# Kernel tuning notes

Hardware: AMD Instinct MI355X
Metric: run time of the kernel (lower is better)

The kernel has to match this reference:

```python
import jax, jax.numpy as jnp
import numpy as np

N_NODES = 50000
N_EDGES = 600000
D_NODE_IN = 32
D_EDGE_IN = 16
H = 128
D_OUT = 2
N_PASSES = 5
LN_EPS = 1e-6  # flax LayerNorm default


def _dense(key, fan_in, fan_out, scale=0.05):
    return (jax.random.normal(key, (fan_in, fan_out), dtype=jnp.float32) * scale)


def setup_inputs() -> dict:
    key = jax.random.key(0)
    ks = jax.random.split(key, 16)
    inp = {
        "nodes": jax.random.normal(ks[0], (N_NODES, D_NODE_IN), dtype=jnp.float32),
        "edges": jax.random.normal(ks[1], (N_EDGES, D_EDGE_IN), dtype=jnp.float32),
        "senders": jax.random.randint(ks[2], (N_EDGES,), 0, N_NODES, dtype=jnp.int32),
        "receivers": jax.random.randint(ks[3], (N_EDGES,), 0, N_NODES, dtype=jnp.int32),
        # node encoder ReluMLP [128,128]
        "enc_n_W0": _dense(ks[4], D_NODE_IN, H), "enc_n_b0": jnp.zeros((H,), jnp.float32),
        "enc_n_W1": _dense(ks[5], H, H), "enc_n_b1": jnp.zeros((H,), jnp.float32),
        # edge encoder ReluMLP [128,128]
        "enc_e_W0": _dense(ks[6], D_EDGE_IN, H), "enc_e_b0": jnp.zeros((H,), jnp.float32),
        "enc_e_W1": _dense(ks[7], H, H), "enc_e_b1": jnp.zeros((H,), jnp.float32),
        # weight-tied LinearMessagePassingLayer params
        "W_msg": _dense(ks[8], H + H, H),                 # Dense(no bias) on concat(sender_feat, edge)
        "node_W0": _dense(ks[9], H + H, H), "node_b0": jnp.zeros((H,), jnp.float32),
        "node_W1": _dense(ks[10], H, H), "node_b1": jnp.zeros((H,), jnp.float32),
        "W_node": _dense(ks[11], H, H),                   # residual projection, no bias
        "ln_g": jnp.ones((H,), jnp.float32), "ln_b": jnp.zeros((H,), jnp.float32),
        # node decoder ReluMLP [128,2]
        "dec_W0": _dense(ks[12], H, H), "dec_b0": jnp.zeros((H,), jnp.float32),
        "dec_W1": _dense(ks[13], H, D_OUT), "dec_b1": jnp.zeros((D_OUT,), jnp.float32),
    }
    return inp


def _relu_mlp(x, layers):
    # Dense+ReLU for all but last layer; last layer linear.
    n = len(layers)
    for i, (W, b) in enumerate(layers):
        x = x @ W + b
        if i < n - 1:
            x = jax.nn.relu(x)
    return x


def _layer_norm(x, g, b):
    mu = jnp.mean(x, axis=-1, keepdims=True)
    var = jnp.var(x, axis=-1, keepdims=True)
    return (x - mu) * jax.lax.rsqrt(var + LN_EPS) * g + b


def reference(nodes, edges, senders, receivers,
              enc_n_W0, enc_n_b0, enc_n_W1, enc_n_b1,
              enc_e_W0, enc_e_b0, enc_e_W1, enc_e_b1,
              W_msg, node_W0, node_b0, node_W1, node_b1,
              W_node, ln_g, ln_b,
              dec_W0, dec_b0, dec_W1, dec_b1):
    n = _relu_mlp(nodes, [(enc_n_W0, enc_n_b0), (enc_n_W1, enc_n_b1)])  # [N,H]
    e = _relu_mlp(edges, [(enc_e_W0, enc_e_b0), (enc_e_W1, enc_e_b1)])  # [E,H]
    total_nodes = n.shape[0]

    for _ in range(N_PASSES):  # weight-tied process block
        sender_features = n[senders]                                    # gather [E,H]
        msg_in = jnp.concatenate([sender_features, e], axis=-1)         # [E,2H]
        messages = msg_in @ W_msg                                       # [E,H]
        agg = jax.ops.segment_sum(messages, receivers, num_segments=total_nodes)
        node_in = jnp.concatenate([n, agg], axis=-1)                    # [N,2H]
        nodes_out = _relu_mlp(node_in, [(node_W0, node_b0), (node_W1, node_b1)])
        n = _layer_norm(n @ W_node + nodes_out, ln_g, ln_b)

    return _relu_mlp(n, [(dec_W0, dec_b0), (dec_W1, dec_b1)])           # [N,2]
```

## Files before the change

kernel.cpp:

```cpp
#include <hip/hip_runtime.h>

#define DEVFN __device__ __forceinline__

namespace {

constexpr int NN = 50000;
constexpr int NE = 600000;
constexpr int H  = 128;
constexpr float LN_EPS = 1e-6f;

typedef _Float16 f16x8 __attribute__((ext_vector_type(8)));
typedef _Float16 f16x4 __attribute__((ext_vector_type(4)));
typedef float f32x4 __attribute__((ext_vector_type(4)));

DEVFN void mm_block(const float* xsrow, int pitch, int K,
                    const float* __restrict__ W, int c0, float (&acc)[8][4]) {
  for (int k = 0; k < K; k += 4) {
    float4 w0 = *(const float4*)(W + (size_t)(k + 0) * H + c0);
    float4 w1 = *(const float4*)(W + (size_t)(k + 1) * H + c0);
    float4 w2 = *(const float4*)(W + (size_t)(k + 2) * H + c0);
    float4 w3 = *(const float4*)(W + (size_t)(k + 3) * H + c0);
#pragma unroll
    for (int r = 0; r < 8; ++r) {
      float4 a = *(const float4*)(xsrow + r * pitch + k);
      acc[r][0] += a.x * w0.x; acc[r][0] += a.y * w1.x; acc[r][0] += a.z * w2.x; acc[r][0] += a.w * w3.x;
      acc[r][1] += a.x * w0.y; acc[r][1] += a.y * w1.y; acc[r][1] += a.z * w2.y; acc[r][1] += a.w * w3.y;
      acc[r][2] += a.x * w0.z; acc[r][2] += a.y * w1.z; acc[r][2] += a.z * w2.z; acc[r][2] += a.w * w3.z;
      acc[r][3] += a.x * w0.w; acc[r][3] += a.y * w1.w; acc[r][3] += a.z * w2.w; acc[r][3] += a.w * w3.w;
    }
  }
}

DEVFN void linear_body(const float* __restrict__ x, const float* __restrict__ W,
                       float* __restrict__ y, int r0, int R, int t, float* xs) {
  {
    const int r = t & 31, q = t >> 5;
    int row = r0 + r;
    if (row >= R) row = R - 1;
    const float* src = &x[(size_t)row * H + q * 32];
#pragma unroll
    for (int j = 0; j < 8; ++j)
      *(float4*)&xs[r * 132 + q * 32 + j * 4] = *(const float4*)&src[j * 4];
  }
  __syncthreads();
  const int c0 = (t & 31) * 4;
  const int rbase = (t >> 5) * 8;
  float acc[8][4];
#pragma unroll
  for (int r = 0; r < 8; ++r) { acc[r][0] = 0.f; acc[r][1] = 0.f; acc[r][2] = 0.f; acc[r][3] = 0.f; }
  mm_block(&xs[rbase * 132], 132, H, W, c0, acc);
#pragma unroll
  for (int r = 0; r < 8; ++r) {
    int row = r0 + rbase + r;
    if (row < R)
      *(float4*)&y[(size_t)row * H + c0] =
          make_float4(acc[r][0], acc[r][1], acc[r][2], acc[r][3]);
  }
}

template <int K_IN>
__global__ __launch_bounds__(128) void encoder_kernel(
    const float* __restrict__ x, const float* __restrict__ W0,
    const float* __restrict__ b0, const float* __restrict__ W1,
    const float* __restrict__ b1, _Float16* __restrict__ outp, int R) {
  constexpr int PIN = K_IN + 4;
  __shared__ float xs[32 * PIN];
  __shared__ float hs[32 * 132];
  const int t = threadIdx.x;
  const int r0 = blockIdx.x * 32;

  const int nvec = 32 * K_IN / 4;
  for (int i = t; i < nvec; i += 128) {
    int rr = i / (K_IN / 4);
    int kk = (i % (K_IN / 4)) * 4;
    int row = r0 + rr;
    float4 v = make_float4(0.f, 0.f, 0.f, 0.f);
    if (row < R) v = *(const float4*)&x[(size_t)row * K_IN + kk];
    *(float4*)&xs[rr * PIN + kk] = v;
  }
  __syncthreads();

  const int c0 = (t & 31) * 4;
  const int rbase = (t >> 5) * 8;
  float acc[8][4];
  {
    float4 bb = *(const float4*)&b0[c0];
#pragma unroll
    for (int r = 0; r < 8; ++r) { acc[r][0] = bb.x; acc[r][1] = bb.y; acc[r][2] = bb.z; acc[r][3] = bb.w; }
  }
  mm_block(&xs[rbase * PIN], PIN, K_IN, W0, c0, acc);
#pragma unroll
  for (int r = 0; r < 8; ++r) {
    float4 h;
    h.x = fmaxf(acc[r][0], 0.f); h.y = fmaxf(acc[r][1], 0.f);
    h.z = fmaxf(acc[r][2], 0.f); h.w = fmaxf(acc[r][3], 0.f);
    *(float4*)&hs[(rbase + r) * 132 + c0] = h;
  }
  __syncthreads();
  {
    float4 bb = *(const float4*)&b1[c0];
#pragma unroll
    for (int r = 0; r < 8; ++r) { acc[r][0] = bb.x; acc[r][1] = bb.y; acc[r][2] = bb.z; acc[r][3] = bb.w; }
  }
  mm_block(&hs[rbase * 132], 132, H, W1, c0, acc);
#pragma unroll
  for (int r = 0; r < 8; ++r) {
    int row = r0 + rbase + r;
    if (row < R) {
      f16x4 pk = {(_Float16)acc[r][0], (_Float16)acc[r][1],
                  (_Float16)acc[r][2], (_Float16)acc[r][3]};
      *(f16x4*)&outp[(size_t)row * H + c0] = pk;
    }
  }
}

__global__ __launch_bounds__(128) void fold1_kernel(
    const float* __restrict__ Wb, const float* __restrict__ Wt,
    const float* __restrict__ W0b, float* __restrict__ T,
    float* __restrict__ Wf) {
  __shared__ float xs[32 * 132];
  const float* x = (blockIdx.x < 4) ? Wb : Wt;
  float* y = (blockIdx.x < 4) ? T : Wf;
  linear_body(x, W0b, y, (blockIdx.x & 3) * 32, 128, threadIdx.x, xs);
}

__global__ __launch_bounds__(128) void fold2_kernel(
    const float* __restrict__ W1e, const float* __restrict__ b1e,
    const float* __restrict__ T, float* __restrict__ Wc2,
    float* __restrict__ bc2) {
  __shared__ float xs[32 * 132];
  if (blockIdx.x < 4) {
    linear_body(W1e, T, Wc2, blockIdx.x * 32, 128, threadIdx.x, xs);
  } else {
    int j = threadIdx.x;
    float s = 0.f;
    for (int k = 0; k < H; ++k) s += b1e[k] * T[(size_t)k * H + j];
    bc2[j] = s;
  }
}

__global__ __launch_bounds__(64) void prepack4_kernel(
    const float* __restrict__ s0, const float* __restrict__ s1,
    const float* __restrict__ s2, const float* __restrict__ s3,
    _Float16* __restrict__ pkBase) {
  const int z = blockIdx.z;
  const float* W = (z == 0) ? s0 : (z == 1) ? s1 : (z == 2) ? s2 : s3;
  _Float16* pk = pkBase + (size_t)z * 128 * H;
  const int ks = blockIdx.x, ct = blockIdx.y, l = threadIdx.x;
  const int kbase = ks * 32 + (l >> 4) * 8;
  const int col = ct * 16 + (l & 15);
  _Float16 tmp[8];
#pragma unroll
  for (int j = 0; j < 8; ++j)
    tmp[j] = (_Float16)W[(size_t)(kbase + j) * H + col];
  *(f16x8*)&pk[((size_t)((ks * 8 + ct) * 64) + l) * 8] = *(f16x8*)tmp;
}

__global__ __launch_bounds__(64) void prepack_w0e_kernel(
    const float* __restrict__ W0e, _Float16* __restrict__ pk) {
  const int ct = blockIdx.x, l = threadIdx.x;
  const int quad = l >> 4;
  const int col = ct * 16 + (l & 15);
  _Float16 tmp[8];
#pragma unroll
  for (int j = 0; j < 8; ++j) {
    int k = quad * 8 + j;
    tmp[j] = (quad < 2) ? (_Float16)W0e[(size_t)k * H + col] : (_Float16)0.f;
  }
  *(f16x8*)&pk[((size_t)(ct * 64) + l) * 8] = *(f16x8*)tmp;
}

__global__ __launch_bounds__(256) void hist_kernel(const int* __restrict__ recv,
                                                   int* __restrict__ cnt) {
  int i = blockIdx.x * 256 + threadIdx.x;
  if (i < NE) atomicAdd(&cnt[recv[i]], 1);
}

__global__ __launch_bounds__(256) void scan1_kernel(const int* __restrict__ cnt,
                                                    int* __restrict__ excl,
                                                    int* __restrict__ part) {
  __shared__ int s[256];
  int t = threadIdx.x;
  int i = blockIdx.x * 256 + t;
  int v = (i < NN) ? cnt[i] : 0;
  s[t] = v;
  __syncthreads();
  for (int off = 1; off < 256; off <<= 1) {
    int x = (t >= off) ? s[t - off] : 0;
    __syncthreads();
    s[t] += x;
    __syncthreads();
  }
  if (i < NN) excl[i] = s[t] - v;
  if (t == 255) part[blockIdx.x] = s[255];
}

__global__ __launch_bounds__(256) void scan2_kernel(int* __restrict__ part, int nb) {
  __shared__ int s[256];
  int t = threadIdx.x;
  int v = (t < nb) ? part[t] : 0;
  s[t] = v;
  __syncthreads();
  for (int off = 1; off < 256; off <<= 1) {
    int x = (t >= off) ? s[t - off] : 0;
    __syncthreads();
    s[t] += x;
    __syncthreads();
  }
  if (t < nb) part[t] = s[t] - v;
}

__global__ __launch_bounds__(256) void scan3_kernel(int* __restrict__ excl,
                                                    const int* __restrict__ part,
                                                    int* __restrict__ cursor) {
  int i = blockIdx.x * 256 + threadIdx.x;
  if (i < NN) {
    int e = excl[i] + part[i >> 8];
    excl[i] = e;
    cursor[i] = e;
  }
}

__global__ __launch_bounds__(256) void scatter_permute_kernel(
    const int* __restrict__ senders, const int* __restrict__ recv,
    int* __restrict__ cursor, const float* __restrict__ edges,
    int* __restrict__ sendp, _Float16* __restrict__ edgesP16) {
  const int t = threadIdx.x;
  const int i = blockIdx.x * 64 + (t >> 2);
  if (i >= NE) return;
  const int sub = t & 3;
  int pos = 0;
  if (sub == 0) pos = atomicAdd(&cursor[recv[i]], 1);
  pos = __shfl(pos, (t & 63) & ~3);
  if (sub == 0) sendp[pos] = senders[i];
  float4 v = *(const float4*)&edges[(size_t)i * 16 + sub * 4];
  f16x4 h = {(_Float16)v.x, (_Float16)v.y, (_Float16)v.z, (_Float16)v.w};
  *(f16x4*)&edgesP16[(size_t)pos * 16 + sub * 4] = h;
}

__global__ __launch_bounds__(256) void hs_mfma_kernel(
    const _Float16* __restrict__ edgesP16, const int* __restrict__ start,
    const int* __restrict__ endc, const _Float16* __restrict__ pkW0e,
    const float* __restrict__ b0e, float* __restrict__ Hs) {
  const int t = threadIdx.x;
  const int wave = t >> 6, lane = t & 63;
  const int v = blockIdx.x * 4 + wave;
  const int quad = lane >> 4, m16 = lane & 15;
  const int j0 = start[v];
  const int deg = endc[v] - j0;

  float binit[8];
#pragma unroll
  for (int ct = 0; ct < 8; ++ct) binit[ct] = b0e[ct * 16 + m16];
  f16x8 bfrag[8];
#pragma unroll
  for (int ct = 0; ct < 8; ++ct)
    bfrag[ct] = *(const f16x8*)&pkW0e[((size_t)(ct * 64) + lane) * 8];

  float rsum[8][4];
#pragma unroll
  for (int ct = 0; ct < 8; ++ct)
#pragma unroll
    for (int q = 0; q < 4; ++q) rsum[ct][q] = 0.f;

  for (int base = 0; base < deg; base += 16) {
    f16x8 a = {};
    if (quad < 2 && base + m16 < deg)
      a = *(const f16x8*)&edgesP16[(size_t)(j0 + base + m16) * 16 + quad * 8];
#pragma unroll
    for (int ct = 0; ct < 8; ++ct) {
      f32x4 acc = (f32x4){binit[ct], binit[ct], binit[ct], binit[ct]};
      acc = __builtin_amdgcn_mfma_f32_16x16x32_f16(a, bfrag[ct], acc, 0, 0, 0);
#pragma unroll
      for (int q = 0; q < 4; ++q) {
        int row = quad * 4 + q;
        float hv = fmaxf(acc[q], 0.f);
        rsum[ct][q] += (base + row < deg) ? hv : 0.f;
      }
    }
  }
#pragma unroll
  for (int ct = 0; ct < 8; ++ct) {
    float s = (rsum[ct][0] + rsum[ct][1]) + (rsum[ct][2] + rsum[ct][3]);
    s += __shfl_xor(s, 16);
    s += __shfl_xor(s, 32);
    if (lane < 16) Hs[(size_t)v * H + ct * 16 + lane] = s;
  }
}

__global__ __launch_bounds__(128) void blinpack_kernel(
    const float* __restrict__ Hs, const float* __restrict__ Wc2,
    const float* __restrict__ bc2, const int* __restrict__ start,
    const int* __restrict__ endc, _Float16* __restrict__ B2pk) {
  __shared__ float xs[32 * 132];
  const int t = threadIdx.x;
  const int r0 = blockIdx.x * 32;
  {
    const int r = t & 31, q = t >> 5;
    int row = r0 + r;
    if (row >= NN) row = NN - 1;
    const float* src = &Hs[(size_t)row * H + q * 32];
#pragma unroll
    for (int j = 0; j < 8; ++j)
      *(float4*)&xs[r * 132 + q * 32 + j * 4] = *(const float4*)&src[j * 4];
  }
  __syncthreads();
  const int c0 = (t & 31) * 4;
  const int rbase = (t >> 5) * 8;
  const float4 bc4 = *(const float4*)&bc2[c0];
  float acc[8][4];
#pragma unroll
  for (int r = 0; r < 8; ++r) {
    int row = r0 + rbase + r;
    if (row >= NN) row = NN - 1;
    float deg = (float)(endc[row] - start[row]);
    acc[r][0] = deg * bc4.x; acc[r][1] = deg * bc4.y;
    acc[r][2] = deg * bc4.z; acc[r][3] = deg * bc4.w;
  }
  mm_block(&xs[rbase * 132], 132, H, Wc2, c0, acc);
  __syncthreads();
#pragma unroll
  for (int r = 0; r < 8; ++r)
    *(float4*)&xs[(rbase + r) * 132 + c0] =
        make_float4(acc[r][0], acc[r][1], acc[r][2], acc[r][3]);
  __syncthreads();
  const int half = t >> 6, l = t & 63;
  const int tile = blockIdx.x * 2 + half;
  const int rb = half * 16 + (l >> 4) * 4;
  const int col = l & 15;
  _Float16 tmp[32];
#pragma unroll
  for (int ct = 0; ct < 8; ++ct)
#pragma unroll
    for (int q = 0; q < 4; ++q)
      tmp[ct * 4 + q] = (_Float16)xs[(rb + q) * 132 + ct * 16 + col];
  _Float16* dst = &B2pk[((size_t)tile * 64 + l) * 32];
#pragma unroll
  for (int i = 0; i < 4; ++i)
    *(f16x8*)(dst + i * 8) = *(f16x8*)(tmp + i * 8);
}

__global__ __launch_bounds__(256) void gather_kernel(
    const _Float16* __restrict__ n16, const int* __restrict__ start,
    const int* __restrict__ endc, const int* __restrict__ sendp,
    _Float16* __restrict__ S) {
  const int t = threadIdx.x;
  const int v = blockIdx.x * 4 + (t >> 6);
  const int lane = t & 63;
  const int grp = lane >> 4;
  const int c = (lane & 15) * 8;
  float a[8] = {0.f, 0.f, 0.f, 0.f, 0.f, 0.f, 0.f, 0.f};
  const int e = endc[v];
  int j = start[v];
  for (; j + 7 < e; j += 8) {
    int s0 = sendp[j + grp];
    int s1 = sendp[j + 4 + grp];
    f16x8 p0 = *(const f16x8*)&n16[(size_t)s0 * H + c];
    f16x8 p1 = *(const f16x8*)&n16[(size_t)s1 * H + c];
#pragma unroll
    for (int i = 0; i < 8; ++i) a[i] += (float)p0[i] + (float)p1[i];
  }
  for (; j < e; j += 4) {
    int jj = j + grp;
    if (jj < e) {
      int s0 = sendp[jj];
      f16x8 p0 = *(const f16x8*)&n16[(size_t)s0 * H + c];
#pragma unroll
      for (int i = 0; i < 8; ++i) a[i] += (float)p0[i];
    }
  }
#pragma unroll
  for (int i = 0; i < 8; ++i) {
    a[i] += __shfl_xor(a[i], 16);
    a[i] += __shfl_xor(a[i], 32);
  }
  if (lane < 16) {
    f16x8 o;
#pragma unroll
    for (int i = 0; i < 8; ++i) o[i] = (_Float16)a[i];
    *(f16x8*)&S[(size_t)v * H + c] = o;
  }
}

__global__ __launch_bounds__(256) void node_mfma_kernel(
    const _Float16* __restrict__ n16, const _Float16* __restrict__ S16,
    const _Float16* __restrict__ B2pk,
    const _Float16* __restrict__ pkW0t, const _Float16* __restrict__ pkWf,
    const float* __restrict__ b0,
    const _Float16* __restrict__ pkW1, const _Float16* __restrict__ pkWn,
    const float* __restrict__ b1,
    const float* __restrict__ ln_g, const float* __restrict__ ln_b,
    _Float16* __restrict__ nout) {
  __shared__ _Float16 lds[4][16 * 136];
  const int t = threadIdx.x;
  const int wave = t >> 6, lane = t & 63;
  const int row0 = blockIdx.x * 64 + wave * 16;
  const int quad = lane >> 4, m16 = lane & 15;
  _Float16* hlds = &lds[wave][0];

  int arow = row0 + m16;
  if (arow >= NN) arow = NN - 1;
  const _Float16* nrow = &n16[(size_t)arow * H + quad * 8];
  const _Float16* srow = &S16[(size_t)arow * H + quad * 8];
  f16x8 an[4], as[4];
#pragma unroll
  for (int ks = 0; ks < 4; ++ks) {
    an[ks] = *(const f16x8*)(nrow + ks * 32);
    as[ks] = *(const f16x8*)(srow + ks * 32);
  }

  const int tile = blockIdx.x * 4 + wave;
  const _Float16* b2l = &B2pk[((size_t)tile * 64 + lane) * 32];
  f32x4 acc[8];
#pragma unroll
  for (int ct = 0; ct < 8; ++ct) {
    float bb = b0[ct * 16 + m16];
    f16x4 bv = *(const f16x4*)(b2l + ct * 4);
    acc[ct] = (f32x4){bb + (float)bv[0], bb + (float)bv[1],
                      bb + (float)bv[2], bb + (float)bv[3]};
  }
#pragma unroll
  for (int ks = 0; ks < 4; ++ks) {
    const _Float16* bp0 = pkW0t + ((size_t)ks * 8 * 64 + lane) * 8;
    const _Float16* bpf = pkWf + ((size_t)ks * 8 * 64 + lane) * 8;
#pragma unroll
    for (int ct = 0; ct < 8; ++ct) {
      f16x8 bw0 = *(const f16x8*)(bp0 + ct * 512);
      acc[ct] = __builtin_amdgcn_mfma_f32_16x16x32_f16(an[ks], bw0, acc[ct], 0, 0, 0);
      f16x8 bwf = *(const f16x8*)(bpf + ct * 512);
      acc[ct] = __builtin_amdgcn_mfma_f32_16x16x32_f16(as[ks], bwf, acc[ct], 0, 0, 0);
    }
  }
#pragma unroll
  for (int ct = 0; ct < 8; ++ct) {
#pragma unroll
    for (int q = 0; q < 4; ++q)
      hlds[(quad * 4 + q) * 136 + ct * 16 + m16] =
          (_Float16)fmaxf(acc[ct][q], 0.f);
  }
  __syncthreads();

  const _Float16* hrow = &hlds[m16 * 136 + quad * 8];
  f32x4 acc2[8];
#pragma unroll
  for (int ct = 0; ct < 8; ++ct) {
    float bb = b1[ct * 16 + m16];
    acc2[ct] = (f32x4){bb, bb, bb, bb};
  }
#pragma unroll
  for (int ks = 0; ks < 4; ++ks) {
    f16x8 ah = *(const f16x8*)(hrow + ks * 32);
    const _Float16* bp1 = pkW1 + ((size_t)ks * 8 * 64 + lane) * 8;
    const _Float16* bpn = pkWn + ((size_t)ks * 8 * 64 + lane) * 8;
#pragma unroll
    for (int ct = 0; ct < 8; ++ct) {
      f16x8 b1f = *(const f16x8*)(bp1 + ct * 512);
      acc2[ct] = __builtin_amdgcn_mfma_f32_16x16x32_f16(ah, b1f, acc2[ct], 0, 0, 0);
      f16x8 bnf = *(const f16x8*)(bpn + ct * 512);
      acc2[ct] = __builtin_amdgcn_mfma_f32_16x16x32_f16(an[ks], bnf, acc2[ct], 0, 0, 0);
    }
  }

  float gv[8], bv[8];
#pragma unroll
  for (int ct = 0; ct < 8; ++ct) {
    gv[ct] = ln_g[ct * 16 + m16];
    bv[ct] = ln_b[ct * 16 + m16];
  }
  __syncthreads();
#pragma unroll
  for (int q = 0; q < 4; ++q) {
    float s1 = 0.f, s2 = 0.f;
#pragma unroll
    for (int ct = 0; ct < 8; ++ct) {
      float v = acc2[ct][q];
      s1 += v; s2 += v * v;
    }
#pragma unroll
    for (int m = 1; m <= 8; m <<= 1) {
      s1 += __shfl_xor(s1, m);
      s2 += __shfl_xor(s2, m);
    }
    float mu = s1 * (1.f / 128.f);
    float var = s2 * (1.f / 128.f) - mu * mu;
    float rs = rsqrtf(var + LN_EPS);
#pragma unroll
    for (int ct = 0; ct < 8; ++ct) {
      float o = (acc2[ct][q] - mu) * rs * gv[ct] + bv[ct];
      hlds[(quad * 4 + q) * 136 + ct * 16 + m16] = (_Float16)o;
    }
  }
  __syncthreads();

  {
    int lr = lane >> 2;
    int cc = (lane & 3) * 32;
    const _Float16* src = &hlds[lr * 136 + cc];
    int orow = row0 + lr;
    if (orow < NN) {
      _Float16* dst = &nout[(size_t)orow * H + cc];
      *(f16x8*)(dst + 0)  = *(const f16x8*)(src + 0);
      *(f16x8*)(dst + 8)  = *(const f16x8*)(src + 8);
      *(f16x8*)(dst + 16) = *(const f16x8*)(src + 16);
      *(f16x8*)(dst + 24) = *(const f16x8*)(src + 24);
    }
  }
}

__global__ __launch_bounds__(128) void decode_kernel(
    const _Float16* __restrict__ n, const float* __restrict__ W0,
    const float* __restrict__ b0, const float* __restrict__ W1,
    const float* __restrict__ b1, float* __restrict__ out) {
  __shared__ float xs[32 * 132];
  __shared__ float hs[32 * 132];
  const int t = threadIdx.x;
  const int r0 = blockIdx.x * 32;
  {
    const int r = t & 31, q = t >> 5;
    int row = r0 + r;
    if (row >= NN) row = NN - 1;
    const _Float16* src = &n[(size_t)row * H + q * 32];
#pragma unroll
    for (int j = 0; j < 4; ++j) {
      f16x8 v8 = *(const f16x8*)&src[j * 8];
#pragma unroll
      for (int i = 0; i < 8; ++i)
        xs[r * 132 + q * 32 + j * 8 + i] = (float)v8[i];
    }
  }
  __syncthreads();
  const int c0 = (t & 31) * 4;
  const int rbase = (t >> 5) * 8;
  float acc[8][4];
  {
    float4 bb = *(const float4*)&b0[c0];
#pragma unroll
    for (int r = 0; r < 8; ++r) { acc[r][0] = bb.x; acc[r][1] = bb.y; acc[r][2] = bb.z; acc[r][3] = bb.w; }
  }
  mm_block(&xs[rbase * 132], 132, H, W0, c0, acc);
#pragma unroll
  for (int r = 0; r < 8; ++r) {
    float4 h;
    h.x = fmaxf(acc[r][0], 0.f); h.y = fmaxf(acc[r][1], 0.f);
    h.z = fmaxf(acc[r][2], 0.f); h.w = fmaxf(acc[r][3], 0.f);
    *(float4*)&hs[(rbase + r) * 132 + c0] = h;
  }
  __syncthreads();
  if (t < 64) {
    int r = t >> 1, c = t & 1;
    float s = b1[c];
    for (int k = 0; k < H; ++k) s += hs[r * 132 + k] * W1[k * 2 + c];
    int row = r0 + r;
    if (row < NN) out[(size_t)row * 2 + c] = s;
  }
}

__global__ __launch_bounds__(256) void zero_kernel(float4* __restrict__ p, int n4) {
  int i = blockIdx.x * 256 + threadIdx.x;
  if (i < n4) p[i] = make_float4(0.f, 0.f, 0.f, 0.f);
}

}

extern "C" void kernel_launch(void* const* d_in, const int* in_sizes, int n_in,
                              void* d_out, int out_size, void* d_ws, size_t ws_size,
                              hipStream_t stream) {
  const float* nodes     = (const float*)d_in[0];
  const float* edges     = (const float*)d_in[1];
  const int*   senders   = (const int*)d_in[2];
  const int*   receivers = (const int*)d_in[3];
  const float* enc_n_W0 = (const float*)d_in[4];
  const float* enc_n_b0 = (const float*)d_in[5];
  const float* enc_n_W1 = (const float*)d_in[6];
  const float* enc_n_b1 = (const float*)d_in[7];
  const float* enc_e_W0 = (const float*)d_in[8];
  const float* enc_e_b0 = (const float*)d_in[9];
  const float* enc_e_W1 = (const float*)d_in[10];
  const float* enc_e_b1 = (const float*)d_in[11];
  const float* W_msg    = (const float*)d_in[12];
  const float* node_W0  = (const float*)d_in[13];
  const float* node_b0  = (const float*)d_in[14];
  const float* node_W1  = (const float*)d_in[15];
  const float* node_b1  = (const float*)d_in[16];
  const float* W_node   = (const float*)d_in[17];
  const float* ln_g     = (const float*)d_in[18];
  const float* ln_b     = (const float*)d_in[19];
  const float* dec_W0   = (const float*)d_in[20];
  const float* dec_b0   = (const float*)d_in[21];
  const float* dec_W1   = (const float*)d_in[22];
  const float* dec_b1   = (const float*)d_in[23];
  float* out = (float*)d_out;

  const float* Wt  = W_msg;
  const float* Wb  = W_msg + 128 * H;
  const float* W0t = node_W0;
  const float* W0b = node_W0 + 128 * H;

  const int mfmaBlocks = (NN + 63) / 64;
  const int nTiles     = mfmaBlocks * 4;

  float* Hs     = (float*)d_ws;
  float* T      = Hs + (size_t)NN * H;
  float* Wc2    = T + 128 * H;
  float* Wf32   = Wc2 + 128 * H;
  float* bc2    = Wf32 + 128 * H;
  _Float16* edgesP16 = (_Float16*)(bc2 + 128);
  _Float16* n16a  = edgesP16 + (size_t)NE * 16;
  _Float16* n16b  = n16a + (size_t)NN * H;
  _Float16* S16   = n16b + (size_t)NN * H;
  _Float16* B2pk  = S16 + (size_t)NN * H;
  _Float16* pkAll = B2pk + (size_t)nTiles * 64 * 32;
  _Float16* pkW0t = pkAll;
  _Float16* pkWf  = pkAll + 1 * 128 * H;
  _Float16* pkW1  = pkAll + 2 * 128 * H;
  _Float16* pkWn  = pkAll + 3 * 128 * H;
  _Float16* pkW0e = pkAll + 4 * 128 * H;
  int* cnt    = (int*)(pkW0e + 4096);
  int* excl   = cnt + NN;
  int* cursor = excl + NN;
  int* part   = cursor + NN;
  int* sendp  = part + 256;

  const int nodeBlocks = (NN + 31) / 32;
  const int scanBlocks = (NN + 255) / 256;
  const int neBlocks   = (NE + 255) / 256;

  zero_kernel<<<(NN / 4 + 255) / 256, 256, 0, stream>>>((float4*)cnt, NN / 4);
  hist_kernel<<<neBlocks, 256, 0, stream>>>(receivers, cnt);
  scan1_kernel<<<scanBlocks, 256, 0, stream>>>(cnt, excl, part);
  scan2_kernel<<<1, 256, 0, stream>>>(part, scanBlocks);
  scan3_kernel<<<scanBlocks, 256, 0, stream>>>(excl, part, cursor);
  scatter_permute_kernel<<<(NE + 63) / 64, 256, 0, stream>>>(
      senders, receivers, cursor, edges, sendp, edgesP16);

  fold1_kernel<<<8, 128, 0, stream>>>(Wb, Wt, W0b, T, Wf32);
  fold2_kernel<<<5, 128, 0, stream>>>(enc_e_W1, enc_e_b1, T, Wc2, bc2);
  prepack4_kernel<<<dim3(4, 8, 4), 64, 0, stream>>>(W0t, Wf32, node_W1, W_node, pkAll);
  prepack_w0e_kernel<<<8, 64, 0, stream>>>(enc_e_W0, pkW0e);

  encoder_kernel<32><<<nodeBlocks, 128, 0, stream>>>(
      nodes, enc_n_W0, enc_n_b0, enc_n_W1, enc_n_b1, n16a, NN);
  hs_mfma_kernel<<<NN / 4, 256, 0, stream>>>(
      edgesP16, excl, cursor, pkW0e, enc_e_b0, Hs);
  blinpack_kernel<<<nodeBlocks, 128, 0, stream>>>(Hs, Wc2, bc2, excl, cursor, B2pk);

  _Float16* ncur = n16a;
  _Float16* nnxt = n16b;
  for (int p = 0; p < 5; ++p) {
    gather_kernel<<<NN / 4, 256, 0, stream>>>(ncur, excl, cursor, sendp, S16);
    node_mfma_kernel<<<mfmaBlocks, 256, 0, stream>>>(
        ncur, S16, B2pk, pkW0t, pkWf, node_b0, pkW1, pkWn, node_b1,
        ln_g, ln_b, nnxt);
    _Float16* tmp = ncur; ncur = nnxt; nnxt = tmp;
  }

  decode_kernel<<<nodeBlocks, 128, 0, stream>>>(ncur, dec_W0, dec_b0, dec_W1, dec_b1, out);
}
```

Baseline: 628.0 us.

## Move node encoder, blinpack and decoder matmuls onto fp16 MFMA

```diff
diff --git a/kernel.cpp b/kernel.cpp
--- a/kernel.cpp
+++ b/kernel.cpp
@@ -55,62 +55,6 @@
     if (row < R)
       *(float4*)&y[(size_t)row * H + c0] =
           make_float4(acc[r][0], acc[r][1], acc[r][2], acc[r][3]);
-  }
-}
-
-template <int K_IN>
-__global__ __launch_bounds__(128) void encoder_kernel(
-    const float* __restrict__ x, const float* __restrict__ W0,
-    const float* __restrict__ b0, const float* __restrict__ W1,
-    const float* __restrict__ b1, _Float16* __restrict__ outp, int R) {
-  constexpr int PIN = K_IN + 4;
-  __shared__ float xs[32 * PIN];
-  __shared__ float hs[32 * 132];
-  const int t = threadIdx.x;
-  const int r0 = blockIdx.x * 32;
-
-  const int nvec = 32 * K_IN / 4;
-  for (int i = t; i < nvec; i += 128) {
-    int rr = i / (K_IN / 4);
-    int kk = (i % (K_IN / 4)) * 4;
-    int row = r0 + rr;
-    float4 v = make_float4(0.f, 0.f, 0.f, 0.f);
-    if (row < R) v = *(const float4*)&x[(size_t)row * K_IN + kk];
-    *(float4*)&xs[rr * PIN + kk] = v;
-  }
-  __syncthreads();
-
-  const int c0 = (t & 31) * 4;
-  const int rbase = (t >> 5) * 8;
-  float acc[8][4];
-  {
-    float4 bb = *(const float4*)&b0[c0];
-#pragma unroll
-    for (int r = 0; r < 8; ++r) { acc[r][0] = bb.x; acc[r][1] = bb.y; acc[r][2] = bb.z; acc[r][3] = bb.w; }
-  }
-  mm_block(&xs[rbase * PIN], PIN, K_IN, W0, c0, acc);
-#pragma unroll
-  for (int r = 0; r < 8; ++r) {
-    float4 h;
-    h.x = fmaxf(acc[r][0], 0.f); h.y = fmaxf(acc[r][1], 0.f);
-    h.z = fmaxf(acc[r][2], 0.f); h.w = fmaxf(acc[r][3], 0.f);
-    *(float4*)&hs[(rbase + r) * 132 + c0] = h;
-  }
-  __syncthreads();
-  {
-    float4 bb = *(const float4*)&b1[c0];
-#pragma unroll
-    for (int r = 0; r < 8; ++r) { acc[r][0] = bb.x; acc[r][1] = bb.y; acc[r][2] = bb.z; acc[r][3] = bb.w; }
-  }
-  mm_block(&hs[rbase * 132], 132, H, W1, c0, acc);
-#pragma unroll
-  for (int r = 0; r < 8; ++r) {
-    int row = r0 + rbase + r;
-    if (row < R) {
-      f16x4 pk = {(_Float16)acc[r][0], (_Float16)acc[r][1],
-                  (_Float16)acc[r][2], (_Float16)acc[r][3]};
-      *(f16x4*)&outp[(size_t)row * H + c0] = pk;
-    }
   }
 }
 
@@ -139,12 +83,14 @@
   }
 }
 
-__global__ __launch_bounds__(64) void prepack4_kernel(
+__global__ __launch_bounds__(64) void prepack7_kernel(
     const float* __restrict__ s0, const float* __restrict__ s1,
     const float* __restrict__ s2, const float* __restrict__ s3,
-    _Float16* __restrict__ pkBase) {
+    const float* __restrict__ s4, const float* __restrict__ s5,
+    const float* __restrict__ s6, _Float16* __restrict__ pkBase) {
   const int z = blockIdx.z;
-  const float* W = (z == 0) ? s0 : (z == 1) ? s1 : (z == 2) ? s2 : s3;
+  const float* W = (z == 0) ? s0 : (z == 1) ? s1 : (z == 2) ? s2 :
+                   (z == 3) ? s3 : (z == 4) ? s4 : (z == 5) ? s5 : s6;
   _Float16* pk = pkBase + (size_t)z * 128 * H;
   const int ks = blockIdx.x, ct = blockIdx.y, l = threadIdx.x;
   const int kbase = ks * 32 + (l >> 4) * 8;
@@ -167,6 +113,18 @@
     int k = quad * 8 + j;
     tmp[j] = (quad < 2) ? (_Float16)W0e[(size_t)k * H + col] : (_Float16)0.f;
   }
+  *(f16x8*)&pk[((size_t)(ct * 64) + l) * 8] = *(f16x8*)tmp;
+}
+
+__global__ __launch_bounds__(64) void prepack_k32_kernel(
+    const float* __restrict__ W, _Float16* __restrict__ pk) {
+  const int ct = blockIdx.x, l = threadIdx.x;
+  const int quad = l >> 4;
+  const int col = ct * 16 + (l & 15);
+  _Float16 tmp[8];
+#pragma unroll
+  for (int j = 0; j < 8; ++j)
+    tmp[j] = (_Float16)W[(size_t)(quad * 8 + j) * H + col];
   *(f16x8*)&pk[((size_t)(ct * 64) + l) * 8] = *(f16x8*)tmp;
 }
 
@@ -238,6 +196,79 @@
   *(f16x4*)&edgesP16[(size_t)pos * 16 + sub * 4] = h;
 }
 
+__global__ __launch_bounds__(256) void encoder_mfma_kernel(
+    const float* __restrict__ x, const float* __restrict__ b0,
+    const float* __restrict__ b1, const _Float16* __restrict__ pkEW0,
+    const _Float16* __restrict__ pkEW1, _Float16* __restrict__ outp) {
+  __shared__ _Float16 lds[4][16 * 136];
+  const int t = threadIdx.x;
+  const int wave = t >> 6, lane = t & 63;
+  const int row0 = blockIdx.x * 64 + wave * 16;
+  const int quad = lane >> 4, m16 = lane & 15;
+  _Float16* hlds = &lds[wave][0];
+
+  int arow = row0 + m16;
+  if (arow >= NN) arow = NN - 1;
+  f16x8 a0;
+  {
+    const float* src = &x[(size_t)arow * 32 + quad * 8];
+    float4 v0 = *(const float4*)(src);
+    float4 v1 = *(const float4*)(src + 4);
+    a0[0] = (_Float16)v0.x; a0[1] = (_Float16)v0.y;
+    a0[2] = (_Float16)v0.z; a0[3] = (_Float16)v0.w;
+    a0[4] = (_Float16)v1.x; a0[5] = (_Float16)v1.y;
+    a0[6] = (_Float16)v1.z; a0[7] = (_Float16)v1.w;
+  }
+#pragma unroll
+  for (int ct = 0; ct < 8; ++ct) {
+    float bb = b0[ct * 16 + m16];
+    f32x4 acc = (f32x4){bb, bb, bb, bb};
+    acc = __builtin_amdgcn_mfma_f32_16x16x32_f16(
+        a0, *(const f16x8*)&pkEW0[((size_t)(ct * 64) + lane) * 8], acc, 0, 0, 0);
+#pragma unroll
+    for (int q = 0; q < 4; ++q)
+      hlds[(quad * 4 + q) * 136 + ct * 16 + m16] = (_Float16)fmaxf(acc[q], 0.f);
+  }
+  __syncthreads();
+  const _Float16* hrow = &hlds[m16 * 136 + quad * 8];
+  f16x8 ah[4];
+#pragma unroll
+  for (int ks = 0; ks < 4; ++ks) ah[ks] = *(const f16x8*)(hrow + ks * 32);
+  f32x4 acc2[8];
+#pragma unroll
+  for (int ct = 0; ct < 8; ++ct) {
+    float bb = b1[ct * 16 + m16];
+    acc2[ct] = (f32x4){bb, bb, bb, bb};
+  }
+#pragma unroll
+  for (int ks = 0; ks < 4; ++ks) {
+    const _Float16* bp = pkEW1 + ((size_t)ks * 8 * 64 + lane) * 8;
+#pragma unroll
+    for (int ct = 0; ct < 8; ++ct)
+      acc2[ct] = __builtin_amdgcn_mfma_f32_16x16x32_f16(
+          ah[ks], *(const f16x8*)(bp + ct * 512), acc2[ct], 0, 0, 0);
+  }
+  __syncthreads();
+#pragma unroll
+  for (int ct = 0; ct < 8; ++ct)
+#pragma unroll
+    for (int q = 0; q < 4; ++q)
+      hlds[(quad * 4 + q) * 136 + ct * 16 + m16] = (_Float16)acc2[ct][q];
+  __syncthreads();
+  {
+    int lr = lane >> 2, cc = (lane & 3) * 32;
+    int orow = row0 + lr;
+    if (orow < NN) {
+      const _Float16* src = &hlds[lr * 136 + cc];
+      _Float16* dst = &outp[(size_t)orow * H + cc];
+      *(f16x8*)(dst + 0)  = *(const f16x8*)(src + 0);
+      *(f16x8*)(dst + 8)  = *(const f16x8*)(src + 8);
+      *(f16x8*)(dst + 16) = *(const f16x8*)(src + 16);
+      *(f16x8*)(dst + 24) = *(const f16x8*)(src + 24);
+    }
+  }
+}
+
 __global__ __launch_bounds__(256) void hs_mfma_kernel(
     const _Float16* __restrict__ edgesP16, const int* __restrict__ start,
     const int* __restrict__ endc, const _Float16* __restrict__ pkW0e,
@@ -288,53 +319,56 @@
   }
 }
 
-__global__ __launch_bounds__(128) void blinpack_kernel(
-    const float* __restrict__ Hs, const float* __restrict__ Wc2,
+__global__ __launch_bounds__(256) void blinpack_mfma_kernel(
+    const float* __restrict__ Hs, const _Float16* __restrict__ pkWc2,
     const float* __restrict__ bc2, const int* __restrict__ start,
     const int* __restrict__ endc, _Float16* __restrict__ B2pk) {
-  __shared__ float xs[32 * 132];
   const int t = threadIdx.x;
-  const int r0 = blockIdx.x * 32;
-  {
-    const int r = t & 31, q = t >> 5;
-    int row = r0 + r;
-    if (row >= NN) row = NN - 1;
-    const float* src = &Hs[(size_t)row * H + q * 32];
-#pragma unroll
-    for (int j = 0; j < 8; ++j)
-      *(float4*)&xs[r * 132 + q * 32 + j * 4] = *(const float4*)&src[j * 4];
-  }
-  __syncthreads();
-  const int c0 = (t & 31) * 4;
-  const int rbase = (t >> 5) * 8;
-  const float4 bc4 = *(const float4*)&bc2[c0];
-  float acc[8][4];
-#pragma unroll
-  for (int r = 0; r < 8; ++r) {
-    int row = r0 + rbase + r;
-    if (row >= NN) row = NN - 1;
-    float deg = (float)(endc[row] - start[row]);
-    acc[r][0] = deg * bc4.x; acc[r][1] = deg * bc4.y;
-    acc[r][2] = deg * bc4.z; acc[r][3] = deg * bc4.w;
-  }
-  mm_block(&xs[rbase * 132], 132, H, Wc2, c0, acc);
-  __syncthreads();
-#pragma unroll
-  for (int r = 0; r < 8; ++r)
-    *(float4*)&xs[(rbase + r) * 132 + c0] =
-        make_float4(acc[r][0], acc[r][1], acc[r][2], acc[r][3]);
-  __syncthreads();
-  const int half = t >> 6, l = t & 63;
-  const int tile = blockIdx.x * 2 + half;
-  const int rb = half * 16 + (l >> 4) * 4;
-  const int col = l & 15;
+  const int wave = t >> 6, lane = t & 63;
+  const int tile = blockIdx.x * 4 + wave;
+  const int row0 = tile * 16;
+  const int quad = lane >> 4, m16 = lane & 15;
+  int arow = row0 + m16;
+  if (arow >= NN) arow = NN - 1;
+  f16x8 ah[4];
+#pragma unroll
+  for (int ks = 0; ks < 4; ++ks) {
+    const float* src = &Hs[(size_t)arow * H + ks * 32 + quad * 8];
+    float4 v0 = *(const float4*)src;
+    float4 v1 = *(const float4*)(src + 4);
+    f16x8 a;
+    a[0] = (_Float16)v0.x; a[1] = (_Float16)v0.y;
+    a[2] = (_Float16)v0.z; a[3] = (_Float16)v0.w;
+    a[4] = (_Float16)v1.x; a[5] = (_Float16)v1.y;
+    a[6] = (_Float16)v1.z; a[7] = (_Float16)v1.w;
+    ah[ks] = a;
+  }
+  float degq[4];
+#pragma unroll
+  for (int q = 0; q < 4; ++q) {
+    int r = row0 + quad * 4 + q;
+    degq[q] = (r < NN) ? (float)(endc[r] - start[r]) : 0.f;
+  }
+  f32x4 acc[8];
+#pragma unroll
+  for (int ct = 0; ct < 8; ++ct) {
+    float bcv = bc2[ct * 16 + m16];
+    acc[ct] = (f32x4){degq[0] * bcv, degq[1] * bcv, degq[2] * bcv, degq[3] * bcv};
+  }
+#pragma unroll
+  for (int ks = 0; ks < 4; ++ks) {
+    const _Float16* bp = pkWc2 + ((size_t)ks * 8 * 64 + lane) * 8;
+#pragma unroll
+    for (int ct = 0; ct < 8; ++ct)
+      acc[ct] = __builtin_amdgcn_mfma_f32_16x16x32_f16(
+          ah[ks], *(const f16x8*)(bp + ct * 512), acc[ct], 0, 0, 0);
+  }
   _Float16 tmp[32];
 #pragma unroll
   for (int ct = 0; ct < 8; ++ct)
 #pragma unroll
-    for (int q = 0; q < 4; ++q)
-      tmp[ct * 4 + q] = (_Float16)xs[(rb + q) * 132 + ct * 16 + col];
-  _Float16* dst = &B2pk[((size_t)tile * 64 + l) * 32];
+    for (int q = 0; q < 4; ++q) tmp[ct * 4 + q] = (_Float16)acc[ct][q];
+  _Float16* dst = &B2pk[((size_t)tile * 64 + lane) * 32];
 #pragma unroll
   for (int i = 0; i < 4; ++i)
     *(f16x8*)(dst + i * 8) = *(f16x8*)(tmp + i * 8);
@@ -507,51 +541,62 @@
   }
 }
 
-__global__ __launch_bounds__(128) void decode_kernel(
-    const _Float16* __restrict__ n, const float* __restrict__ W0,
-    const float* __restrict__ b0, const float* __restrict__ W1,
+__global__ __launch_bounds__(256) void decode_mfma_kernel(
+    const _Float16* __restrict__ n, const float* __restrict__ b0,
+    const _Float16* __restrict__ pkDW0, const float* __restrict__ W1,
     const float* __restrict__ b1, float* __restrict__ out) {
-  __shared__ float xs[32 * 132];
-  __shared__ float hs[32 * 132];
   const int t = threadIdx.x;
-  const int r0 = blockIdx.x * 32;
-  {
-    const int r = t & 31, q = t >> 5;
-    int row = r0 + r;
-    if (row >= NN) row = NN - 1;
-    const _Float16* src = &n[(size_t)row * H + q * 32];
-#pragma unroll
-    for (int j = 0; j < 4; ++j) {
-      f16x8 v8 = *(const f16x8*)&src[j * 8];
-#pragma unroll
-      for (int i = 0; i < 8; ++i)
-        xs[r * 132 + q * 32 + j * 8 + i] = (float)v8[i];
-    }
-  }
-  __syncthreads();
-  const int c0 = (t & 31) * 4;
-  const int rbase = (t >> 5) * 8;
-  float acc[8][4];
-  {
-    float4 bb = *(const float4*)&b0[c0];
-#pragma unroll
-    for (int r = 0; r < 8; ++r) { acc[r][0] = bb.x; acc[r][1] = bb.y; acc[r][2] = bb.z; acc[r][3] = bb.w; }
-  }
-  mm_block(&xs[rbase * 132], 132, H, W0, c0, acc);
-#pragma unroll
-  for (int r = 0; r < 8; ++r) {
-    float4 h;
-    h.x = fmaxf(acc[r][0], 0.f); h.y = fmaxf(acc[r][1], 0.f);
-    h.z = fmaxf(acc[r][2], 0.f); h.w = fmaxf(acc[r][3], 0.f);
-    *(float4*)&hs[(rbase + r) * 132 + c0] = h;
-  }
-  __syncthreads();
-  if (t < 64) {
-    int r = t >> 1, c = t & 1;
-    float s = b1[c];
-    for (int k = 0; k < H; ++k) s += hs[r * 132 + k] * W1[k * 2 + c];
-    int row = r0 + r;
-    if (row < NN) out[(size_t)row * 2 + c] = s;
+  const int wave = t >> 6, lane = t & 63;
+  const int row0 = blockIdx.x * 64 + wave * 16;
+  const int quad = lane >> 4, m16 = lane & 15;
+  int arow = row0 + m16;
+  if (arow >= NN) arow = NN - 1;
+  const _Float16* nrow = &n[(size_t)arow * H + quad * 8];
+  f16x8 an[4];
+#pragma unroll
+  for (int ks = 0; ks < 4; ++ks) an[ks] = *(const f16x8*)(nrow + ks * 32);
+  f32x4 acc[8];
+#pragma unroll
+  for (int ct = 0; ct < 8; ++ct) {
+    float bb = b0[ct * 16 + m16];
+    acc[ct] = (f32x4){bb, bb, bb, bb};
+  }
+#pragma unroll
+  for (int ks = 0; ks < 4; ++ks) {
+    const _Float16* bp = pkDW0 + ((size_t)ks * 8 * 64 + lane) * 8;
+#pragma unroll
+    for (int ct = 0; ct < 8; ++ct)
+      acc[ct] = __builtin_amdgcn_mfma_f32_16x16x32_f16(
+          an[ks], *(const f16x8*)(bp + ct * 512), acc[ct], 0, 0, 0);
+  }
+  float s0[4] = {0.f, 0.f, 0.f, 0.f}, s1[4] = {0.f, 0.f, 0.f, 0.f};
+#pragma unroll
+  for (int ct = 0; ct < 8; ++ct) {
+    const float2 w = *(const float2*)&W1[(size_t)(ct * 16 + m16) * 2];
+#pragma unroll
+    for (int q = 0; q < 4; ++q) {
+      float h = fmaxf(acc[ct][q], 0.f);
+      s0[q] += h * w.x;
+      s1[q] += h * w.y;
+    }
+  }
+#pragma unroll
+  for (int q = 0; q < 4; ++q) {
+#pragma unroll
+    for (int m = 1; m <= 8; m <<= 1) {
+      s0[q] += __shfl_xor(s0[q], m);
+      s1[q] += __shfl_xor(s1[q], m);
+    }
+  }
+  if (m16 == 0) {
+#pragma unroll
+    for (int q = 0; q < 4; ++q) {
+      int r = row0 + quad * 4 + q;
+      if (r < NN) {
+        out[(size_t)r * 2 + 0] = s0[q] + b1[0];
+        out[(size_t)r * 2 + 1] = s1[q] + b1[1];
+      }
+    }
   }
 }
 
@@ -614,14 +659,17 @@
   _Float16* pkWf  = pkAll + 1 * 128 * H;
   _Float16* pkW1  = pkAll + 2 * 128 * H;
   _Float16* pkWn  = pkAll + 3 * 128 * H;
-  _Float16* pkW0e = pkAll + 4 * 128 * H;
-  int* cnt    = (int*)(pkW0e + 4096);
+  _Float16* pkEW1 = pkAll + 4 * 128 * H;
+  _Float16* pkDW0 = pkAll + 5 * 128 * H;
+  _Float16* pkWc2 = pkAll + 6 * 128 * H;
+  _Float16* pkW0e = pkAll + 7 * 128 * H;
+  _Float16* pkEW0 = pkW0e + 4096;
+  int* cnt    = (int*)(pkEW0 + 4096);
   int* excl   = cnt + NN;
   int* cursor = excl + NN;
   int* part   = cursor + NN;
   int* sendp  = part + 256;
 
-  const int nodeBlocks = (NN + 31) / 32;
   const int scanBlocks = (NN + 255) / 256;
   const int neBlocks   = (NE + 255) / 256;
 
@@ -635,14 +683,17 @@
 
   fold1_kernel<<<8, 128, 0, stream>>>(Wb, Wt, W0b, T, Wf32);
   fold2_kernel<<<5, 128, 0, stream>>>(enc_e_W1, enc_e_b1, T, Wc2, bc2);
-  prepack4_kernel<<<dim3(4, 8, 4), 64, 0, stream>>>(W0t, Wf32, node_W1, W_node, pkAll);
+  prepack7_kernel<<<dim3(4, 8, 7), 64, 0, stream>>>(
+      W0t, Wf32, node_W1, W_node, enc_n_W1, dec_W0, Wc2, pkAll);
   prepack_w0e_kernel<<<8, 64, 0, stream>>>(enc_e_W0, pkW0e);
-
-  encoder_kernel<32><<<nodeBlocks, 128, 0, stream>>>(
-      nodes, enc_n_W0, enc_n_b0, enc_n_W1, enc_n_b1, n16a, NN);
+  prepack_k32_kernel<<<8, 64, 0, stream>>>(enc_n_W0, pkEW0);
+
+  encoder_mfma_kernel<<<mfmaBlocks, 256, 0, stream>>>(
+      nodes, enc_n_b0, enc_n_b1, pkEW0, pkEW1, n16a);
   hs_mfma_kernel<<<NN / 4, 256, 0, stream>>>(
       edgesP16, excl, cursor, pkW0e, enc_e_b0, Hs);
-  blinpack_kernel<<<nodeBlocks, 128, 0, stream>>>(Hs, Wc2, bc2, excl, cursor, B2pk);
+  blinpack_mfma_kernel<<<mfmaBlocks, 256, 0, stream>>>(
+      Hs, pkWc2, bc2, excl, cursor, B2pk);
 
   _Float16* ncur = n16a;
   _Float16* nnxt = n16b;
@@ -654,5 +705,6 @@
     _Float16* tmp = ncur; ncur = nnxt; nnxt = tmp;
   }
 
-  decode_kernel<<<nodeBlocks, 128, 0, stream>>>(ncur, dec_W0, dec_b0, dec_W1, dec_b1, out);
-}
+  decode_mfma_kernel<<<mfmaBlocks, 256, 0, stream>>>(
+      ncur, dec_b0, pkDW0, dec_W1, dec_b1, out);
+}
```

After: 559.9 us. 10.8% less time.
